# Kernel optimization log

Hardware: AMD Instinct MI355X
Metric: run time of the kernel (lower is better)

Reference implementation:

```python
import jax, jax.numpy as jnp
import numpy as np

DROPOUT_P = 0.5
LEAKY_ALPHA = 0.2
NEG_INF = -9e15


def setup_inputs() -> dict:
    key = jax.random.key(0)
    k_h, k_adj, k_W, k_a = jax.random.split(key, 4)
    B, N, F_in, F_out = 8, 2048, 128, 64
    h = jax.random.normal(k_h, (B, N, F_in), dtype=jnp.float32)
    adj = jax.random.randint(k_adj, (B, N, N), 0, 2, dtype=jnp.int32)
    W = jax.random.normal(k_W, (F_in, F_out), dtype=jnp.float32)
    a = jax.random.normal(k_a, (2 * F_out, 1), dtype=jnp.float32)
    return {"h": h, "adj": adj, "W": W, "a": a}


def reference(h, adj, W, a):
    F_out = W.shape[1]
    Wh = jnp.einsum('bni,io->bno', h, W)                 # [B,N,F_out]
    Wh1 = Wh @ a[:F_out]                                  # [B,N,1]
    Wh2 = Wh @ a[F_out:]                                  # [B,N,1]
    e = jax.nn.leaky_relu(Wh1 + jnp.swapaxes(Wh2, 1, 2), LEAKY_ALPHA)  # [B,N,N]
    att = jnp.where(adj > 0, e, NEG_INF)
    att = jax.nn.softmax(att, axis=2)
    # F.dropout(attention, 0.5) with training=True (torch default)
    keep = jax.random.bernoulli(jax.random.key(42), 1.0 - DROPOUT_P, att.shape)
    att = att * keep.astype(att.dtype) / (1.0 - DROPOUT_P)
    embedding = jnp.matmul(att, Wh)                       # [B,N,F_out]
    return embedding
```

## Files before the change

### kernel.cpp

```cpp
#include <hip/hip_runtime.h>
#include <stdint.h>

#define NB   8
#define NN   2048
#define FIN  128
#define FOUT 64
#define NEGINF (-9e15f)
#define MAXS 512

__device__ __forceinline__ uint32_t rotl32(uint32_t x, uint32_t r) {
  return (x << r) | (x >> (32u - r));
}

__device__ __forceinline__ void threefry_0_42(uint32_t x0, uint32_t x1,
                                              uint32_t& o0, uint32_t& o1) {
  const uint32_t k0 = 0u, k1 = 42u;
  const uint32_t k2 = 0x1BD11BDAu ^ k0 ^ k1;
  x0 += k0; x1 += k1;
#define TFR(r) { x0 += x1; x1 = rotl32(x1, r); x1 ^= x0; }
  TFR(13u) TFR(15u) TFR(26u) TFR(6u)   x0 += k1; x1 += k2 + 1u;
  TFR(17u) TFR(29u) TFR(16u) TFR(24u)  x0 += k2; x1 += k0 + 2u;
  TFR(13u) TFR(15u) TFR(26u) TFR(6u)   x0 += k0; x1 += k1 + 3u;
  TFR(17u) TFR(29u) TFR(16u) TFR(24u)  x0 += k1; x1 += k2 + 4u;
  TFR(13u) TFR(15u) TFR(26u) TFR(6u)   x0 += k2; x1 += k0 + 5u;
#undef TFR
  o0 = x0; o1 = x1;
}

__device__ __forceinline__ bool keep_bit(uint32_t v) {
  uint32_t o0, o1;
  threefry_0_42(0u, v, o0, o1);
  return !((o0 ^ o1) >> 31);
}

__global__ __launch_bounds__(256) void wh_kernel(
    const float* __restrict__ h, const float* __restrict__ W,
    const float* __restrict__ a, float* __restrict__ Wh,
    float* __restrict__ Wh1, float* __restrict__ Wh2) {
  __shared__ __align__(16) float wLds[FIN * FOUT];
  __shared__ __align__(16) float hLds[4][FIN];
  const int t = threadIdx.x;
  const int wv = t >> 6, lane = t & 63;
  {
    const float4* W4 = reinterpret_cast<const float4*>(W);
    float4* wL4 = reinterpret_cast<float4*>(wLds);
    for (int idx = t; idx < FIN * FOUT / 4; idx += 256) wL4[idx] = W4[idx];
  }
  const int row = blockIdx.x * 4 + wv;
  {
    float2 v = *reinterpret_cast<const float2*>(&h[(size_t)row * FIN + lane * 2]);
    hLds[wv][lane * 2]     = v.x;
    hLds[wv][lane * 2 + 1] = v.y;
  }
  __syncthreads();
  float acc = 0.f;
#pragma unroll 8
  for (int k = 0; k < FIN; ++k) acc += hLds[wv][k] * wLds[k * FOUT + lane];
  Wh[(size_t)row * FOUT + lane] = acc;
  float x1 = acc * a[lane];
  float x2 = acc * a[FOUT + lane];
#pragma unroll
  for (int off = 32; off >= 1; off >>= 1) {
    x1 += __shfl_xor(x1, off);
    x2 += __shfl_xor(x2, off);
  }
  if (lane == 0) { Wh1[row] = x1; Wh2[row] = x2; }
}

__global__ __launch_bounds__(256) void attn_kernel(
    const int* __restrict__ adj, const float* __restrict__ Wh,
    const float* __restrict__ Wh1, const float* __restrict__ Wh2,
    float* __restrict__ out) {
  __shared__ float mredA[2][4], sredA[2][4];
  __shared__ int cnt[2];
  __shared__ int   survJ[2][MAXS];
  __shared__ float survP[2][MAXS];
  __shared__ float accL[2][4][FOUT];

  const int i = blockIdx.x & (NN - 1);
  const int b = blockIdx.x >> 11;
  const int b2 = b + 4;
  const int t = threadIdx.x;
  const int wv = t >> 6, lane = t & 63;

  const float wh1_0 = Wh1[b * NN + i];
  const float wh1_1 = Wh1[b2 * NN + i];
  const size_t adjBase0 = ((size_t)(b * NN) + i) * NN;
  const size_t adjBase1 = ((size_t)(b2 * NN) + i) * NN;

  float e0[8], e1[8];
  float m0 = -3.0e38f, m1 = -3.0e38f;
#pragma unroll
  for (int it = 0; it < 2; ++it) {
    const int j = it * 1024 + t * 4;
    const int4   av0 = *reinterpret_cast<const int4*>(adj + adjBase0 + j);
    const int4   av1 = *reinterpret_cast<const int4*>(adj + adjBase1 + j);
    const float4 w0 = *reinterpret_cast<const float4*>(Wh2 + (size_t)b * NN + j);
    const float4 w1 = *reinterpret_cast<const float4*>(Wh2 + (size_t)b2 * NN + j);
    const int aa0[4] = {av0.x, av0.y, av0.z, av0.w};
    const int aa1[4] = {av1.x, av1.y, av1.z, av1.w};
    const float ww0[4] = {w0.x, w0.y, w0.z, w0.w};
    const float ww1[4] = {w1.x, w1.y, w1.z, w1.w};
#pragma unroll
    for (int e = 0; e < 4; ++e) {
      float x = wh1_0 + ww0[e];
      x = (x < 0.f) ? 0.2f * x : x;
      x = (aa0[e] > 0) ? x : NEGINF;
      e0[it * 4 + e] = x;
      m0 = fmaxf(m0, x);
      float y = wh1_1 + ww1[e];
      y = (y < 0.f) ? 0.2f * y : y;
      y = (aa1[e] > 0) ? y : NEGINF;
      e1[it * 4 + e] = y;
      m1 = fmaxf(m1, y);
    }
  }
#pragma unroll
  for (int off = 1; off < 64; off <<= 1) {
    m0 = fmaxf(m0, __shfl_xor(m0, off));
    m1 = fmaxf(m1, __shfl_xor(m1, off));
  }
  if (lane == 0) { mredA[0][wv] = m0; mredA[1][wv] = m1; }
  if (t < 2) cnt[t] = 0;
  __syncthreads();
  m0 = fmaxf(fmaxf(mredA[0][0], mredA[0][1]), fmaxf(mredA[0][2], mredA[0][3]));
  m1 = fmaxf(fmaxf(mredA[1][0], mredA[1][1]), fmaxf(mredA[1][2], mredA[1][3]));

  float s0 = 0.f, s1 = 0.f;
#pragma unroll
  for (int k = 0; k < 8; ++k) {
    const int j = (k >> 2) * 1024 + t * 4 + (k & 3);
    float p = __expf(e0[k] - m0);
    s0 += p;
    if (p > 1e-10f) {
      const int idx = atomicAdd(&cnt[0], 1);
      if (idx < MAXS) { survJ[0][idx] = j; survP[0][idx] = p; }
    }
    p = __expf(e1[k] - m1);
    s1 += p;
    if (p > 1e-10f) {
      const int idx = atomicAdd(&cnt[1], 1);
      if (idx < MAXS) { survJ[1][idx] = j; survP[1][idx] = p; }
    }
  }
#pragma unroll
  for (int off = 1; off < 64; off <<= 1) {
    s0 += __shfl_xor(s0, off);
    s1 += __shfl_xor(s1, off);
  }
  if (lane == 0) { sredA[0][wv] = s0; sredA[1][wv] = s1; }
  __syncthreads();
  s0 = sredA[0][0] + sredA[0][1] + sredA[0][2] + sredA[0][3];
  s1 = sredA[1][0] + sredA[1][1] + sredA[1][2] + sredA[1][3];
  const float inv0 = 2.0f / s0;
  const float inv1 = 2.0f / s1;
  const int c0 = min(cnt[0], MAXS), c1 = min(cnt[1], MAXS);

  for (int idx = t; idx < c0; idx += 256) {
    const uint32_t v = ((uint32_t)b << 22) | ((uint32_t)i << 11) | (uint32_t)survJ[0][idx];
    survP[0][idx] = keep_bit(v) ? survP[0][idx] * inv0 : 0.f;
  }
  for (int idx = t; idx < c1; idx += 256) {
    const uint32_t v = ((uint32_t)b2 << 22) | ((uint32_t)i << 11) | (uint32_t)survJ[1][idx];
    survP[1][idx] = keep_bit(v) ? survP[1][idx] * inv1 : 0.f;
  }
  __syncthreads();

  float acc0 = 0.f, acc1 = 0.f;
  for (int idx = wv; idx < c0; idx += 4) {
    const float c = survP[0][idx];
    if (c != 0.f)
      acc0 += c * Wh[((size_t)(b * NN + survJ[0][idx])) * FOUT + lane];
  }
  for (int idx = wv; idx < c1; idx += 4) {
    const float c = survP[1][idx];
    if (c != 0.f)
      acc1 += c * Wh[((size_t)(b2 * NN + survJ[1][idx])) * FOUT + lane];
  }
  accL[0][wv][lane] = acc0;
  accL[1][wv][lane] = acc1;
  __syncthreads();
  if (t < 128) {
    const int bb = t >> 6, f = t & 63;
    const float r = accL[bb][0][f] + accL[bb][1][f] + accL[bb][2][f] + accL[bb][3][f];
    const int bo = (bb == 0) ? b : b2;
    out[((size_t)bo * NN + i) * FOUT + f] = r;
  }
}

extern "C" void kernel_launch(void* const* d_in, const int* in_sizes, int n_in,
                              void* d_out, int out_size, void* d_ws, size_t ws_size,
                              hipStream_t stream) {
  const float* h   = (const float*)d_in[0];
  const int*   adj = (const int*)d_in[1];
  const float* W   = (const float*)d_in[2];
  const float* a   = (const float*)d_in[3];
  float* out = (float*)d_out;
  float* ws  = (float*)d_ws;

  float* Wh  = ws;
  float* Wh1 = ws + (size_t)NB * NN * FOUT;
  float* Wh2 = Wh1 + NB * NN;

  wh_kernel<<<dim3((NB * NN) / 4), dim3(256), 0, stream>>>(h, W, a, Wh, Wh1, Wh2);
  attn_kernel<<<dim3((NB / 2) * NN), dim3(256), 0, stream>>>(adj, Wh, Wh1, Wh2, out);
}
```

Measured before the change: 57.27 us.

## Compute softmax max from masked Wh2 and skip exp below threshold

Because leaky ReLU is monotonic, the row max is now derived from the max of masked Wh2 values rather than from every activated score, and exp plus atomics run only for entries within a fixed margin of that max. The attention kernel also loads 8 contiguous adj elements per thread, and wh_kernel computes 16 rows per block with 4 rows per wave, so the W tile in LDS is loaded once per 16 rows instead of once per 4. The fixed 116 threshold depends on the leaky slope and the 1e-10 cutoff, and in the negative region (slope 0.2) it may drop terms that the exact softmax would keep.

```diff
diff --git a/kernel.cpp b/kernel.cpp
--- a/kernel.cpp
+++ b/kernel.cpp
@@ -5,7 +5,6 @@
 #define NN   2048
 #define FIN  128
 #define FOUT 64
-#define NEGINF (-9e15f)
 #define MAXS 512
 
 __device__ __forceinline__ uint32_t rotl32(uint32_t x, uint32_t r) {
@@ -38,40 +37,50 @@
     const float* __restrict__ a, float* __restrict__ Wh,
     float* __restrict__ Wh1, float* __restrict__ Wh2) {
   __shared__ __align__(16) float wLds[FIN * FOUT];
-  __shared__ __align__(16) float hLds[4][FIN];
+  __shared__ __align__(16) float hLds[16][FIN];
   const int t = threadIdx.x;
   const int wv = t >> 6, lane = t & 63;
+  const int rbase = blockIdx.x * 16;
   {
     const float4* W4 = reinterpret_cast<const float4*>(W);
     float4* wL4 = reinterpret_cast<float4*>(wLds);
     for (int idx = t; idx < FIN * FOUT / 4; idx += 256) wL4[idx] = W4[idx];
-  }
-  const int row = blockIdx.x * 4 + wv;
-  {
-    float2 v = *reinterpret_cast<const float2*>(&h[(size_t)row * FIN + lane * 2]);
-    hLds[wv][lane * 2]     = v.x;
-    hLds[wv][lane * 2 + 1] = v.y;
-  }
-  __syncthreads();
-  float acc = 0.f;
-#pragma unroll 8
-  for (int k = 0; k < FIN; ++k) acc += hLds[wv][k] * wLds[k * FOUT + lane];
-  Wh[(size_t)row * FOUT + lane] = acc;
-  float x1 = acc * a[lane];
-  float x2 = acc * a[FOUT + lane];
-#pragma unroll
-  for (int off = 32; off >= 1; off >>= 1) {
-    x1 += __shfl_xor(x1, off);
-    x2 += __shfl_xor(x2, off);
-  }
-  if (lane == 0) { Wh1[row] = x1; Wh2[row] = x2; }
+    const float4* h4 = reinterpret_cast<const float4*>(h + (size_t)rbase * FIN);
+    float4* hL4 = reinterpret_cast<float4*>(&hLds[0][0]);
+    for (int idx = t; idx < 16 * FIN / 4; idx += 256) hL4[idx] = h4[idx];
+  }
+  __syncthreads();
+  const int r0 = wv * 4;
+  float acc0 = 0.f, acc1 = 0.f, acc2 = 0.f, acc3 = 0.f;
+#pragma unroll 4
+  for (int k = 0; k < FIN; ++k) {
+    const float w = wLds[k * FOUT + lane];
+    acc0 += hLds[r0 + 0][k] * w;
+    acc1 += hLds[r0 + 1][k] * w;
+    acc2 += hLds[r0 + 2][k] * w;
+    acc3 += hLds[r0 + 3][k] * w;
+  }
+  const float a1 = a[lane], a2 = a[FOUT + lane];
+  float accs[4] = {acc0, acc1, acc2, acc3};
+#pragma unroll
+  for (int r = 0; r < 4; ++r) {
+    const int row = rbase + r0 + r;
+    Wh[(size_t)row * FOUT + lane] = accs[r];
+    float x1 = accs[r] * a1, x2 = accs[r] * a2;
+#pragma unroll
+    for (int off = 32; off >= 1; off >>= 1) {
+      x1 += __shfl_xor(x1, off);
+      x2 += __shfl_xor(x2, off);
+    }
+    if (lane == 0) { Wh1[row] = x1; Wh2[row] = x2; }
+  }
 }
 
 __global__ __launch_bounds__(256) void attn_kernel(
     const int* __restrict__ adj, const float* __restrict__ Wh,
     const float* __restrict__ Wh1, const float* __restrict__ Wh2,
     float* __restrict__ out) {
-  __shared__ float mredA[2][4], sredA[2][4];
+  __shared__ float redA[2][4];
   __shared__ int cnt[2];
   __shared__ int   survJ[2][MAXS];
   __shared__ float survP[2][MAXS];
@@ -87,60 +96,71 @@
   const float wh1_1 = Wh1[b2 * NN + i];
   const size_t adjBase0 = ((size_t)(b * NN) + i) * NN;
   const size_t adjBase1 = ((size_t)(b2 * NN) + i) * NN;
-
-  float e0[8], e1[8];
-  float m0 = -3.0e38f, m1 = -3.0e38f;
-#pragma unroll
-  for (int it = 0; it < 2; ++it) {
-    const int j = it * 1024 + t * 4;
-    const int4   av0 = *reinterpret_cast<const int4*>(adj + adjBase0 + j);
-    const int4   av1 = *reinterpret_cast<const int4*>(adj + adjBase1 + j);
-    const float4 w0 = *reinterpret_cast<const float4*>(Wh2 + (size_t)b * NN + j);
-    const float4 w1 = *reinterpret_cast<const float4*>(Wh2 + (size_t)b2 * NN + j);
-    const int aa0[4] = {av0.x, av0.y, av0.z, av0.w};
-    const int aa1[4] = {av1.x, av1.y, av1.z, av1.w};
-    const float ww0[4] = {w0.x, w0.y, w0.z, w0.w};
-    const float ww1[4] = {w1.x, w1.y, w1.z, w1.w};
-#pragma unroll
-    for (int e = 0; e < 4; ++e) {
-      float x = wh1_0 + ww0[e];
+  const int j0 = t * 8;
+
+  float ww0[8], ww1[8];
+  float mW0 = -3.0e38f, mW1 = -3.0e38f;
+  {
+    const int4   a0a = *reinterpret_cast<const int4*>(adj + adjBase0 + j0);
+    const int4   a0b = *reinterpret_cast<const int4*>(adj + adjBase0 + j0 + 4);
+    const int4   a1a = *reinterpret_cast<const int4*>(adj + adjBase1 + j0);
+    const int4   a1b = *reinterpret_cast<const int4*>(adj + adjBase1 + j0 + 4);
+    const float4 w0a = *reinterpret_cast<const float4*>(Wh2 + (size_t)b * NN + j0);
+    const float4 w0b = *reinterpret_cast<const float4*>(Wh2 + (size_t)b * NN + j0 + 4);
+    const float4 w1a = *reinterpret_cast<const float4*>(Wh2 + (size_t)b2 * NN + j0);
+    const float4 w1b = *reinterpret_cast<const float4*>(Wh2 + (size_t)b2 * NN + j0 + 4);
+    const int aa0[8] = {a0a.x, a0a.y, a0a.z, a0a.w, a0b.x, a0b.y, a0b.z, a0b.w};
+    const int aa1[8] = {a1a.x, a1a.y, a1a.z, a1a.w, a1b.x, a1b.y, a1b.z, a1b.w};
+    const float vv0[8] = {w0a.x, w0a.y, w0a.z, w0a.w, w0b.x, w0b.y, w0b.z, w0b.w};
+    const float vv1[8] = {w1a.x, w1a.y, w1a.z, w1a.w, w1b.x, w1b.y, w1b.z, w1b.w};
+#pragma unroll
+    for (int e = 0; e < 8; ++e) {
+      ww0[e] = (aa0[e] > 0) ? vv0[e] : -1.0e30f;
+      mW0 = fmaxf(mW0, ww0[e]);
+      ww1[e] = (aa1[e] > 0) ? vv1[e] : -1.0e30f;
+      mW1 = fmaxf(mW1, ww1[e]);
+    }
+  }
+#pragma unroll
+  for (int off = 1; off < 64; off <<= 1) {
+    mW0 = fmaxf(mW0, __shfl_xor(mW0, off));
+    mW1 = fmaxf(mW1, __shfl_xor(mW1, off));
+  }
+  if (lane == 0) { redA[0][wv] = mW0; redA[1][wv] = mW1; }
+  if (t < 2) cnt[t] = 0;
+  __syncthreads();
+  mW0 = fmaxf(fmaxf(redA[0][0], redA[0][1]), fmaxf(redA[0][2], redA[0][3]));
+  mW1 = fmaxf(fmaxf(redA[1][0], redA[1][1]), fmaxf(redA[1][2], redA[1][3]));
+
+  const float me0_arg = wh1_0 + mW0;
+  const float me1_arg = wh1_1 + mW1;
+  const float me0 = (me0_arg < 0.f) ? 0.2f * me0_arg : me0_arg;
+  const float me1 = (me1_arg < 0.f) ? 0.2f * me1_arg : me1_arg;
+  const float thr0 = mW0 - 116.f;
+  const float thr1 = mW1 - 116.f;
+
+  float s0 = 0.f, s1 = 0.f;
+#pragma unroll
+  for (int k = 0; k < 8; ++k) {
+    if (ww0[k] > thr0) {
+      float x = wh1_0 + ww0[k];
       x = (x < 0.f) ? 0.2f * x : x;
-      x = (aa0[e] > 0) ? x : NEGINF;
-      e0[it * 4 + e] = x;
-      m0 = fmaxf(m0, x);
-      float y = wh1_1 + ww1[e];
+      const float p = __expf(x - me0);
+      s0 += p;
+      if (p > 1e-10f) {
+        const int idx = atomicAdd(&cnt[0], 1);
+        if (idx < MAXS) { survJ[0][idx] = j0 + k; survP[0][idx] = p; }
+      }
+    }
+    if (ww1[k] > thr1) {
+      float y = wh1_1 + ww1[k];
       y = (y < 0.f) ? 0.2f * y : y;
-      y = (aa1[e] > 0) ? y : NEGINF;
-      e1[it * 4 + e] = y;
-      m1 = fmaxf(m1, y);
-    }
-  }
-#pragma unroll
-  for (int off = 1; off < 64; off <<= 1) {
-    m0 = fmaxf(m0, __shfl_xor(m0, off));
-    m1 = fmaxf(m1, __shfl_xor(m1, off));
-  }
-  if (lane == 0) { mredA[0][wv] = m0; mredA[1][wv] = m1; }
-  if (t < 2) cnt[t] = 0;
-  __syncthreads();
-  m0 = fmaxf(fmaxf(mredA[0][0], mredA[0][1]), fmaxf(mredA[0][2], mredA[0][3]));
-  m1 = fmaxf(fmaxf(mredA[1][0], mredA[1][1]), fmaxf(mredA[1][2], mredA[1][3]));
-
-  float s0 = 0.f, s1 = 0.f;
-#pragma unroll
-  for (int k = 0; k < 8; ++k) {
-    const int j = (k >> 2) * 1024 + t * 4 + (k & 3);
-    float p = __expf(e0[k] - m0);
-    s0 += p;
-    if (p > 1e-10f) {
-      const int idx = atomicAdd(&cnt[0], 1);
-      if (idx < MAXS) { survJ[0][idx] = j; survP[0][idx] = p; }
-    }
-    p = __expf(e1[k] - m1);
-    s1 += p;
-    if (p > 1e-10f) {
-      const int idx = atomicAdd(&cnt[1], 1);
-      if (idx < MAXS) { survJ[1][idx] = j; survP[1][idx] = p; }
+      const float p = __expf(y - me1);
+      s1 += p;
+      if (p > 1e-10f) {
+        const int idx = atomicAdd(&cnt[1], 1);
+        if (idx < MAXS) { survJ[1][idx] = j0 + k; survP[1][idx] = p; }
+      }
     }
   }
 #pragma unroll
@@ -148,10 +168,10 @@
     s0 += __shfl_xor(s0, off);
     s1 += __shfl_xor(s1, off);
   }
-  if (lane == 0) { sredA[0][wv] = s0; sredA[1][wv] = s1; }
-  __syncthreads();
-  s0 = sredA[0][0] + sredA[0][1] + sredA[0][2] + sredA[0][3];
-  s1 = sredA[1][0] + sredA[1][1] + sredA[1][2] + sredA[1][3];
+  if (lane == 0) { redA[0][wv] = s0; redA[1][wv] = s1; }
+  __syncthreads();
+  s0 = redA[0][0] + redA[0][1] + redA[0][2] + redA[0][3];
+  s1 = redA[1][0] + redA[1][1] + redA[1][2] + redA[1][3];
   const float inv0 = 2.0f / s0;
   const float inv1 = 2.0f / s1;
   const int c0 = min(cnt[0], MAXS), c1 = min(cnt[1], MAXS);
@@ -202,6 +222,6 @@
   float* Wh1 = ws + (size_t)NB * NN * FOUT;
   float* Wh2 = Wh1 + NB * NN;
 
-  wh_kernel<<<dim3((NB * NN) / 4), dim3(256), 0, stream>>>(h, W, a, Wh, Wh1, Wh2);
+  wh_kernel<<<dim3((NB * NN) / 16), dim3(256), 0, stream>>>(h, W, a, Wh, Wh1, Wh2);
   attn_kernel<<<dim3((NB / 2) * NN), dim3(256), 0, stream>>>(adj, Wh, Wh1, Wh2, out);
 }
```

New measurement: 51.16 us. 1.12x faster.
